# Kernel optimization log

Measured on AMD Instinct MI355X. Metric: run time of the kernel, lower is better.

Reference implementation:

```python
import jax, jax.numpy as jnp
import numpy as np

HIDDEN = 896
N_HEADS = 14
N_KV_HEADS = 2
HEAD_DIM = HIDDEN // N_HEADS  # 64
ROPE_THETA = 1000000.0
B, S = 2, 2048


def setup_inputs() -> dict:
    key = jax.random.key(0)
    ks = jax.random.split(key, 8)
    hidden_states = jax.random.normal(ks[0], (B, S, HIDDEN), dtype=jnp.float32)
    # causal additive mask (1,1,S,S): 0 allowed, -1e9 masked
    causal = jnp.tril(jnp.ones((S, S), dtype=bool))
    attention_mask = jnp.where(causal, 0.0, -1e9).astype(jnp.float32)[None, None]
    sc = 1.0 / np.sqrt(HIDDEN)
    Wq = jax.random.normal(ks[1], (N_HEADS * HEAD_DIM, HIDDEN), dtype=jnp.float32) * sc
    bq = jnp.zeros((N_HEADS * HEAD_DIM,), dtype=jnp.float32)
    Wk = jax.random.normal(ks[2], (N_KV_HEADS * HEAD_DIM, HIDDEN), dtype=jnp.float32) * sc
    bk = jnp.zeros((N_KV_HEADS * HEAD_DIM,), dtype=jnp.float32)
    Wv = jax.random.normal(ks[3], (N_KV_HEADS * HEAD_DIM, HIDDEN), dtype=jnp.float32) * sc
    bv = jnp.zeros((N_KV_HEADS * HEAD_DIM,), dtype=jnp.float32)
    Wo = jax.random.normal(ks[4], (HIDDEN, N_HEADS * HEAD_DIM), dtype=jnp.float32) * sc
    return {"hidden_states": hidden_states, "attention_mask": attention_mask,
            "Wq": Wq, "bq": bq, "Wk": Wk, "bk": bk, "Wv": Wv, "bv": bv, "Wo": Wo}


def _rotate_half(x):
    h = x.shape[-1] // 2
    return jnp.concatenate((-x[..., h:], x[..., :h]), axis=-1)


def _rope_cos_sin(seq_len, dtype):
    inv_freq = 1.0 / (ROPE_THETA ** (jnp.arange(0, HEAD_DIM, 2, dtype=jnp.float32) / HEAD_DIM))
    t = jnp.arange(seq_len, dtype=jnp.float32)
    freqs = jnp.outer(t, inv_freq)                 # [S, D/2]
    emb = jnp.concatenate((freqs, freqs), axis=-1)  # [S, D]
    return jnp.cos(emb).astype(dtype)[None, None], jnp.sin(emb).astype(dtype)[None, None]


def reference(hidden_states, attention_mask, Wq, bq, Wk, bk, Wv, bv, Wo):
    b, s, _ = hidden_states.shape
    groups = N_HEADS // N_KV_HEADS
    q = (hidden_states @ Wq.T + bq).reshape(b, s, N_HEADS, HEAD_DIM).transpose(0, 2, 1, 3)
    k = (hidden_states @ Wk.T + bk).reshape(b, s, N_KV_HEADS, HEAD_DIM).transpose(0, 2, 1, 3)
    v = (hidden_states @ Wv.T + bv).reshape(b, s, N_KV_HEADS, HEAD_DIM).transpose(0, 2, 1, 3)
    cos, sin = _rope_cos_sin(s, q.dtype)
    q = q * cos + _rotate_half(q) * sin
    k = k * cos + _rotate_half(k) * sin
    k = jnp.repeat(k, groups, axis=1)  # GQA expand: [b, H, s, d]
    v = jnp.repeat(v, groups, axis=1)
    scores = jnp.einsum('bhqd,bhkd->bhqk', q, k) / np.sqrt(HEAD_DIM) + attention_mask
    w = jax.nn.softmax(scores.astype(jnp.float32), axis=-1).astype(q.dtype)
    out = jnp.einsum('bhqk,bhkd->bhqd', w, v)
    out = out.transpose(0, 2, 1, 3).reshape(b, s, HIDDEN)
    return out @ Wo.T
```

## Files before the change

kernel.cpp:

```cpp
#include <hip/hip_runtime.h>
#include <hip/hip_bf16.h>

#define BATCH 2
#define SEQ   2048
#define HID   896
#define NH    14
#define NKV   2
#define HDIM  64
#define GRP   7
#define ROWS  (BATCH*SEQ)
#define NQKV  1152

typedef float f32x4 __attribute__((ext_vector_type(4)));
typedef short s16x8 __attribute__((ext_vector_type(8)));
typedef unsigned short u16;

#define MFMA_BF16(a,b,c) __builtin_amdgcn_mfma_f32_16x16x32_bf16((a),(b),(c),0,0,0)

__device__ __forceinline__ u16 f2b(float f) {
  __hip_bfloat16 h = __float2bfloat16(f);
  return __builtin_bit_cast(u16, h);
}
__device__ __forceinline__ float b2f(u16 u) {
  unsigned v = ((unsigned)u) << 16;
  return __builtin_bit_cast(float, v);
}

__device__ __forceinline__ void gload16(const void* g, void* l) {
  __builtin_amdgcn_global_load_lds((const __attribute__((address_space(1))) void*)g,
                                   (__attribute__((address_space(3))) void*)l,
                                   16, 0, 0);
}

__device__ __forceinline__ int chunk_prefix(int qi) {
  if (qi < 32)  return qi;
  if (qi < 64)  return 32 + (qi - 32) * 2;
  if (qi < 96)  return 96 + (qi - 64) * 3;
  return 192 + (qi - 96) * 4;
}

__global__ __launch_bounds__(256) void k_prep(const float* __restrict__ hidden,
                                              const float* __restrict__ Wq,
                                              const float* __restrict__ Wk,
                                              const float* __restrict__ Wv,
                                              const float* __restrict__ Wo,
                                              u16* __restrict__ hidB,
                                              u16* __restrict__ WqkvB,
                                              u16* __restrict__ WoB,
                                              float* __restrict__ ct,
                                              float* __restrict__ st) {
  const int bid = blockIdx.x, t = threadIdx.x;
  if (bid < 5376) {
    const float* src; u16* dst; int i;
    if (bid < 3584)      { src = hidden; dst = hidB;            i = bid*256 + t; }
    else if (bid < 4368) { src = Wq;     dst = WqkvB;           i = (bid-3584)*256 + t; }
    else if (bid < 4480) { src = Wk;     dst = WqkvB + 802816;  i = (bid-4368)*256 + t; }
    else if (bid < 4592) { src = Wv;     dst = WqkvB + 917504;  i = (bid-4480)*256 + t; }
    else                 { src = Wo;     dst = WoB;             i = (bid-4592)*256 + t; }
    float4 v = reinterpret_cast<const float4*>(src)[i];
    ushort4 o = { f2b(v.x), f2b(v.y), f2b(v.z), f2b(v.w) };
    reinterpret_cast<ushort4*>(dst)[i] = o;
  } else {
    const int i = (bid - 5376)*256 + t;
    const int s = i >> 5, fi = i & 31;
    double inv = exp(-(double)fi / 32.0 * log(1.0e6));
    double ang = (double)s * inv;
    ct[i] = (float)cos(ang);
    st[i] = (float)sin(ang);
  }
}

__global__ __launch_bounds__(256) void k_gemm_qkv(const u16* __restrict__ A,
                                                  const u16* __restrict__ Bt,
                                                  const float* __restrict__ bq,
                                                  const float* __restrict__ bk,
                                                  const float* __restrict__ bv,
                                                  const float* __restrict__ ct,
                                                  const float* __restrict__ st,
                                                  u16* __restrict__ Qr,
                                                  u16* __restrict__ Kf,
                                                  u16* __restrict__ Vf) {
  __shared__ __align__(16) u16 lA[2][128 * 32];
  __shared__ __align__(16) u16 lB[2][128 * 32];
  const int K = HID;
  const int t = threadIdx.x;
  const int l = t & 63, w = t >> 6;
  const int lr = l & 15, lg = l >> 4;
  const int wr = w >> 1, wc = w & 1;
  const int bm = blockIdx.x * 128, bn = blockIdx.y * 128;
  const int srow = (l >> 2) & 3;
  const int sslot = (l & 3) ^ srow;
  const int rsw = (lr & 3);

  f32x4 acc[4][4] = {};

#define GSTAGE(buf, k0)                                                          \
  {                                                                              \
    _Pragma("unroll")                                                            \
    for (int i = 0; i < 2; ++i) {                                                \
      const int row = i*64 + w*16 + (l>>2);                                      \
      gload16(A  + (size_t)(bm + row) * K + (k0) + sslot*8,                      \
              (char*)lA[buf] + i*4096 + w*1024);                                 \
      gload16(Bt + (size_t)(bn + row) * K + (k0) + sslot*8,                      \
              (char*)lB[buf] + i*4096 + w*1024);                                 \
    }                                                                            \
  }

  int cur = 0;
  GSTAGE(0, 0);
  __syncthreads();
  for (int k0 = 0; k0 < K; k0 += 32) {
    if (k0 + 32 < K) GSTAGE(cur ^ 1, k0 + 32);
    const u16* lAc = lA[cur];
    const u16* lBc = lB[cur];
    s16x8 af[4], bf[4];
    #pragma unroll
    for (int m = 0; m < 4; ++m)
      af[m] = *(const s16x8*)&lAc[(wr*64 + m*16 + lr)*32 + (lg ^ rsw)*8];
    #pragma unroll
    for (int n = 0; n < 4; ++n)
      bf[n] = *(const s16x8*)&lBc[(wc*64 + n*16 + lr)*32 + (lg ^ rsw)*8];
    #pragma unroll
    for (int m = 0; m < 4; ++m)
      #pragma unroll
      for (int n = 0; n < 4; ++n)
        acc[m][n] = MFMA_BF16(af[m], bf[n], acc[m][n]);
    __syncthreads();
    cur ^= 1;
  }
#undef GSTAGE

  const int hcol = blockIdx.y * 2 + wc;
  const int bsel = bm >> 11;
  const float QSC = 0.125f * 1.44269504088896f;

  if (hcol < 14) {
    u16* qb = Qr + (size_t)(bsel*NH + hcol) * SEQ * HDIM;
    float bia0[2], bia2[2];
    #pragma unroll
    for (int n = 0; n < 2; ++n) {
      bia0[n] = bq[hcol*64 + n*16 + lr];
      bia2[n] = bq[hcol*64 + n*16 + lr + 32];
    }
    #pragma unroll
    for (int m = 0; m < 4; ++m)
      #pragma unroll
      for (int j = 0; j < 4; ++j) {
        const int s = (bm + wr*64 + m*16 + lg*4 + j) & (SEQ - 1);
        #pragma unroll
        for (int n = 0; n < 2; ++n) {
          const int ic = n*16 + lr;
          const float c = ct[s*32 + ic], sv = st[s*32 + ic];
          const float x0 = acc[m][n][j] + bia0[n];
          const float x1 = acc[m][n+2][j] + bia2[n];
          qb[(size_t)s*HDIM + ic]      = f2b((x0*c - x1*sv) * QSC);
          qb[(size_t)s*HDIM + ic + 32] = f2b((x1*c + x0*sv) * QSC);
        }
      }
  } else if (hcol < 16) {
    const int hkk = hcol - 14;
    u16* kp = Kf + (size_t)(bsel*NKV + hkk) * SEQ * HDIM;
    float bia0[2], bia2[2];
    #pragma unroll
    for (int n = 0; n < 2; ++n) {
      bia0[n] = bk[hkk*64 + n*16 + lr];
      bia2[n] = bk[hkk*64 + n*16 + lr + 32];
    }
    #pragma unroll
    for (int m = 0; m < 4; ++m)
      #pragma unroll
      for (int j = 0; j < 4; ++j) {
        const int s = (bm + wr*64 + m*16 + lg*4 + j) & (SEQ - 1);
        #pragma unroll
        for (int n = 0; n < 2; ++n) {
          const int d0 = n*16 + lr;
          const float c = ct[s*32 + d0], sv = st[s*32 + d0];
          const float x0 = acc[m][n][j] + bia0[n];
          const float x1 = acc[m][n+2][j] + bia2[n];
          const int off0 = (s>>4)*1024 + ((d0>>3)*128) + (s&15)*8 + (d0&7);
          kp[off0]       = f2b(x0*c - x1*sv);
          kp[off0 + 512] = f2b(x1*c + x0*sv);
        }
      }
  } else {
    const int hkk = hcol - 16;
    u16* vp = Vf + (size_t)(bsel*NKV + hkk) * SEQ * HDIM;
    float biav[4];
    #pragma unroll
    for (int n = 0; n < 4; ++n) biav[n] = bv[hkk*64 + n*16 + lr];
    #pragma unroll
    for (int m = 0; m < 4; ++m)
      #pragma unroll
      for (int j = 0; j < 4; ++j) {
        const int s = (bm + wr*64 + m*16 + lg*4 + j) & (SEQ - 1);
        const int sbase = (s>>6)*4096 + ((s>>5)&1)*512 + ((s>>3)&3)*128 + (s&7);
        #pragma unroll
        for (int n = 0; n < 4; ++n)
          vp[sbase + n*1024 + lr*8] = f2b(acc[m][n][j] + biav[n]);
      }
  }
}

__global__ __launch_bounds__(256) void k_gemm_o(const u16* __restrict__ A,
                                                const u16* __restrict__ Bt,
                                                float* __restrict__ C,
                                                int N, int K) {
  __shared__ __align__(16) u16 lA[2][128 * 32];
  __shared__ __align__(16) u16 lB[2][128 * 32];
  const int t = threadIdx.x;
  const int l = t & 63, w = t >> 6;
  const int lr = l & 15, lg = l >> 4;
  const int wr = w >> 1, wc = w & 1;
  const int bm = blockIdx.x * 128, bn = blockIdx.y * 128;
  const int srow = (l >> 2) & 3;
  const int sslot = (l & 3) ^ srow;
  const int rsw = (lr & 3);

  f32x4 acc[4][4] = {};

#define GSTAGE(buf, k0)                                                          \
  {                                                                              \
    _Pragma("unroll")                                                            \
    for (int i = 0; i < 2; ++i) {                                                \
      const int row = i*64 + w*16 + (l>>2);                                      \
      gload16(A  + (size_t)(bm + row) * K + (k0) + sslot*8,                      \
              (char*)lA[buf] + i*4096 + w*1024);                                 \
      gload16(Bt + (size_t)(bn + row) * K + (k0) + sslot*8,                      \
              (char*)lB[buf] + i*4096 + w*1024);                                 \
    }                                                                            \
  }

  int cur = 0;
  GSTAGE(0, 0);
  __syncthreads();
  for (int k0 = 0; k0 < K; k0 += 32) {
    if (k0 + 32 < K) GSTAGE(cur ^ 1, k0 + 32);
    const u16* lAc = lA[cur];
    const u16* lBc = lB[cur];
    s16x8 af[4], bf[4];
    #pragma unroll
    for (int m = 0; m < 4; ++m)
      af[m] = *(const s16x8*)&lAc[(wr*64 + m*16 + lr)*32 + (lg ^ rsw)*8];
    #pragma unroll
    for (int n = 0; n < 4; ++n)
      bf[n] = *(const s16x8*)&lBc[(wc*64 + n*16 + lr)*32 + (lg ^ rsw)*8];
    #pragma unroll
    for (int m = 0; m < 4; ++m)
      #pragma unroll
      for (int n = 0; n < 4; ++n)
        acc[m][n] = MFMA_BF16(af[m], bf[n], acc[m][n]);
    __syncthreads();
    cur ^= 1;
  }
#undef GSTAGE

  #pragma unroll
  for (int n = 0; n < 4; ++n) {
    const int col = bn + wc*64 + n*16 + lr;
    #pragma unroll
    for (int m = 0; m < 4; ++m)
      #pragma unroll
      for (int j = 0; j < 4; ++j) {
        const int row = bm + wr*64 + m*16 + lg*4 + j;
        C[(size_t)row * N + col] = acc[m][n][j];
      }
  }
}

__global__ __launch_bounds__(256, 4) void k_attn(const u16* __restrict__ Qr,
                                                 const u16* __restrict__ Kf,
                                                 const u16* __restrict__ Vf,
                                                 u16* __restrict__ pAcc,
                                                 float* __restrict__ pML) {
  __shared__ __align__(16) u16 lP[4][16 * 64];

  const int t = threadIdx.x, l = t & 63, w = t >> 6;
  const int lr = l & 15, lg = l >> 4;
  const int g = blockIdx.x % 7;
  const int u = 319 - blockIdx.x / 7;
  int qi, ci;
  if (u < 32)       { qi = u;                 ci = 0; }
  else if (u < 96)  { qi = 32 + ((u-32)>>1);  ci = (u-32) & 1; }
  else if (u < 192) { const int v = u - 96;  const int q3 = v/3; qi = 64 + q3; ci = v - 3*q3; }
  else              { qi = 96 + ((u-192)>>2); ci = (u-192) & 3; }

  const int bh = g*4 + w;
  const int b = bh / NH, h = bh % NH, hk = h / GRP;
  const int nt = (qi >> 2) + 1;
  const int kt0 = ci * 8;
  const int kt1 = min(nt, kt0 + 8);
  const int dt = nt - 1;
  const int qloc = (qi & 3) * 16;
  const int task = bh*320 + chunk_prefix(qi) + ci;

  const u16* qbase = Qr + ((size_t)((b*NH + h) * SEQ + qi*16 + lr)) * HDIM + lg*8;
  const s16x8 qf0 = *(const s16x8*)qbase;
  const s16x8 qf1 = *(const s16x8*)(qbase + 32);
  const u16* kfp = Kf + (size_t)(b*NKV + hk) * SEQ * HDIM;
  const u16* vfp = Vf + (size_t)(b*NKV + hk) * SEQ * HDIM;

  f32x4 acc[4] = {};
  float lrow[4] = {0.f, 0.f, 0.f, 0.f};

  const int psw = (lr >> 2) << 4;

  for (int kt = kt0; kt < kt1; ++kt) {
    const u16* kbb = kfp + (size_t)kt*4096 + l*8;
    const s16x8 kf0 = *(const s16x8*)(kbb);
    const s16x8 kf1 = *(const s16x8*)(kbb + 512);
    const s16x8 kf2 = *(const s16x8*)(kbb + 1024);
    const s16x8 kf3 = *(const s16x8*)(kbb + 1536);
    const s16x8 kf4 = *(const s16x8*)(kbb + 2048);
    const s16x8 kf5 = *(const s16x8*)(kbb + 2560);
    const s16x8 kf6 = *(const s16x8*)(kbb + 3072);
    const s16x8 kf7 = *(const s16x8*)(kbb + 3584);

    f32x4 sc[4];
    __builtin_amdgcn_s_setprio(1);
    {
      f32x4 z0 = {0.f,0.f,0.f,0.f}, z1 = {0.f,0.f,0.f,0.f};
      f32x4 z2 = {0.f,0.f,0.f,0.f}, z3 = {0.f,0.f,0.f,0.f};
      z0 = MFMA_BF16(qf0, kf0, z0); z0 = MFMA_BF16(qf1, kf1, z0);
      z1 = MFMA_BF16(qf0, kf2, z1); z1 = MFMA_BF16(qf1, kf3, z1);
      z2 = MFMA_BF16(qf0, kf4, z2); z2 = MFMA_BF16(qf1, kf5, z2);
      z3 = MFMA_BF16(qf0, kf6, z3); z3 = MFMA_BF16(qf1, kf7, z3);
      sc[0] = z0; sc[1] = z1; sc[2] = z2; sc[3] = z3;
    }
    __builtin_amdgcn_s_setprio(0);

    const u16* vbb = vfp + (size_t)kt*4096 + l*8;
    const s16x8 vv0 = *(const s16x8*)(vbb);
    const s16x8 vv1 = *(const s16x8*)(vbb + 512);
    const s16x8 vv2 = *(const s16x8*)(vbb + 1024);
    const s16x8 vv3 = *(const s16x8*)(vbb + 1536);
    const s16x8 vv4 = *(const s16x8*)(vbb + 2048);
    const s16x8 vv5 = *(const s16x8*)(vbb + 2560);
    const s16x8 vv6 = *(const s16x8*)(vbb + 3072);
    const s16x8 vv7 = *(const s16x8*)(vbb + 3584);

    if (kt == dt) {
      #pragma unroll
      for (int f = 0; f < 4; ++f)
        #pragma unroll
        for (int j = 0; j < 4; ++j)
          if (f*16 + lr > qloc + lg*4 + j) sc[f][j] = -1.0e9f;
    }

    #pragma unroll
    for (int f = 0; f < 4; ++f)
      #pragma unroll
      for (int j = 0; j < 4; ++j) {
        float p = exp2f(sc[f][j]);
        sc[f][j] = p;
        lrow[j] += p;
      }

    u16* pw = lP[w];
    #pragma unroll
    for (int f = 0; f < 4; ++f)
      #pragma unroll
      for (int j = 0; j < 4; ++j)
        pw[(lg*4 + j)*64 + ((f*16 + lr) ^ (lg << 4))] = f2b(sc[f][j]);
    s16x8 pa0 = *(const s16x8*)&pw[lr*64 + ((lg*8     ) ^ psw)];
    s16x8 pa1 = *(const s16x8*)&pw[lr*64 + ((32 + lg*8) ^ psw)];

    __builtin_amdgcn_s_setprio(1);
    acc[0] = MFMA_BF16(pa0, vv0, acc[0]); acc[0] = MFMA_BF16(pa1, vv1, acc[0]);
    acc[1] = MFMA_BF16(pa0, vv2, acc[1]); acc[1] = MFMA_BF16(pa1, vv3, acc[1]);
    acc[2] = MFMA_BF16(pa0, vv4, acc[2]); acc[2] = MFMA_BF16(pa1, vv5, acc[2]);
    acc[3] = MFMA_BF16(pa0, vv6, acc[3]); acc[3] = MFMA_BF16(pa1, vv7, acc[3]);
    __builtin_amdgcn_s_setprio(0);
  }

  #pragma unroll
  for (int off = 1; off < 16; off <<= 1)
    #pragma unroll
    for (int j = 0; j < 4; ++j)
      lrow[j] += __shfl_xor(lrow[j], off);

  u16* pa = pAcc + (size_t)task * 1024;
  #pragma unroll
  for (int df = 0; df < 4; ++df) {
    ushort4 o = { f2b(acc[df][0]), f2b(acc[df][1]), f2b(acc[df][2]), f2b(acc[df][3]) };
    *reinterpret_cast<ushort4*>(pa + (df*64 + l)*4) = o;
  }
  if (lr == 0) {
    float* ml = pML + task * 32;
    #pragma unroll
    for (int j = 0; j < 4; ++j)
      ml[lg*4 + j] = lrow[j];
  }
}

__global__ __launch_bounds__(256) void k_reduce(const u16* __restrict__ pAcc,
                                                const float* __restrict__ pML,
                                                u16* __restrict__ Ao) {
  __shared__ __align__(16) u16 lT[4][16 * 64];
  const int t = threadIdx.x, l = t & 63, w = t >> 6;
  const int lr = l & 15, lg = l >> 4;
  const int id = blockIdx.x * 4 + w;
  const int qi = id & 127, bh = id >> 7;
  const int b = bh / NH, h = bh % NH;
  const int nch = 1 + (qi >> 5);
  const int base = bh*320 + chunk_prefix(qi);

  float inv[4];
  #pragma unroll
  for (int j = 0; j < 4; ++j) {
    const int r = lg*4 + j;
    const float l0 = pML[(size_t)(base+0)*32 + r];
    const float l1 = (nch > 1) ? pML[(size_t)(base+1)*32 + r] : 0.f;
    const float l2 = (nch > 2) ? pML[(size_t)(base+2)*32 + r] : 0.f;
    const float l3 = (nch > 3) ? pML[(size_t)(base+3)*32 + r] : 0.f;
    inv[j] = 1.0f / (l0 + l1 + l2 + l3);
  }

  u16* lt = lT[w];
  #pragma unroll
  for (int df = 0; df < 4; ++df) {
    const int eo = (df*64 + l)*4;
    ushort4 a0 = *reinterpret_cast<const ushort4*>(pAcc + (size_t)(base+0)*1024 + eo);
    ushort4 a1 = (nch > 1) ? *reinterpret_cast<const ushort4*>(pAcc + (size_t)(base+1)*1024 + eo) : ushort4{0,0,0,0};
    ushort4 a2 = (nch > 2) ? *reinterpret_cast<const ushort4*>(pAcc + (size_t)(base+2)*1024 + eo) : ushort4{0,0,0,0};
    ushort4 a3 = (nch > 3) ? *reinterpret_cast<const ushort4*>(pAcc + (size_t)(base+3)*1024 + eo) : ushort4{0,0,0,0};
    const u16 e0[4] = {a0.x, a0.y, a0.z, a0.w};
    const u16 e1[4] = {a1.x, a1.y, a1.z, a1.w};
    const u16 e2[4] = {a2.x, a2.y, a2.z, a2.w};
    const u16 e3[4] = {a3.x, a3.y, a3.z, a3.w};
    #pragma unroll
    for (int j = 0; j < 4; ++j) {
      float o = (b2f(e0[j]) + b2f(e1[j]) + b2f(e2[j]) + b2f(e3[j])) * inv[j];
      lt[(lg*4 + j)*64 + df*16 + lr] = f2b(o);
    }
  }

  const size_t orow = (size_t)b * SEQ + qi*16;
  #pragma unroll
  for (int i = 0; i < 2; ++i) {
    const int r = i*8 + (l >> 3);
    const s16x8 vrow = *(const s16x8*)&lt[r*64 + (l & 7)*8];
    *(s16x8*)&Ao[(orow + r) * HID + h*64 + (l & 7)*8] = vrow;
  }
}

extern "C" void kernel_launch(void* const* d_in, const int* in_sizes, int n_in,
                              void* d_out, int out_size, void* d_ws, size_t ws_size,
                              hipStream_t stream) {
  const float* hidden = (const float*)d_in[0];
  const float* Wq = (const float*)d_in[2];
  const float* bq = (const float*)d_in[3];
  const float* Wk = (const float*)d_in[4];
  const float* bk = (const float*)d_in[5];
  const float* Wv = (const float*)d_in[6];
  const float* bv = (const float*)d_in[7];
  const float* Wo = (const float*)d_in[8];

  char* ws = (char*)d_ws;
  u16*   hidB  = (u16*)(ws);
  u16*   Ao    = (u16*)(ws);
  u16*   WqkvB = (u16*)(ws + 7340032);
  u16*   WoB   = (u16*)(ws + 9404416);
  u16*   Qr    = (u16*)(ws + 11010048);
  u16*   Kf    = (u16*)(ws + 18350080);
  u16*   Vf    = (u16*)(ws + 19398656);
  float* ct    = (float*)(ws + 20447232);
  float* st    = (float*)(ws + 20709376);
  u16*   pAcc  = (u16*)(ws + 20971520);
  float* pML   = (float*)(ws + 39321600);

  k_prep<<<dim3(5632), dim3(256), 0, stream>>>(hidden, Wq, Wk, Wv, Wo,
                                               hidB, WqkvB, WoB, ct, st);
  k_gemm_qkv<<<dim3(32, 9), dim3(256), 0, stream>>>(hidB, WqkvB, bq, bk, bv,
                                                    ct, st, Qr, Kf, Vf);
  k_attn<<<dim3(2240), dim3(256), 0, stream>>>(Qr, Kf, Vf, pAcc, pML);
  k_reduce<<<dim3(896), dim3(256), 0, stream>>>(pAcc, pML, Ao);
  k_gemm_o<<<dim3(32, 7), dim3(256), 0, stream>>>(Ao, WoB, (float*)d_out, HID, HID);
}
```

Before: 104.3 us.

## Process two 16-row query tiles per wave in attention to reuse K/V loads

Each attention wave now handles 32 query rows (two 16-row MFMA tiles) instead of 16, so every K and V fragment loaded from global memory feeds twice as many MFMAs. The work decomposition, chunk prefix indexing, partial-accumulator layout and the reduce kernel are reworked for 32-row tiles, and the grids are halved. The cost is more registers (8 accumulators, double score fragments), a lower occupancy hint of 3, and fewer blocks to balance across CUs.

```diff
diff --git a/kernel.cpp b/kernel.cpp
--- a/kernel.cpp
+++ b/kernel.cpp
@@ -32,11 +32,15 @@
                                    16, 0, 0);
 }
 
-__device__ __forceinline__ int chunk_prefix(int qi) {
-  if (qi < 32)  return qi;
-  if (qi < 64)  return 32 + (qi - 32) * 2;
-  if (qi < 96)  return 96 + (qi - 64) * 3;
-  return 192 + (qi - 96) * 4;
+__device__ __forceinline__ int S8(int n) {
+  if (n <= 8)  return n;
+  if (n <= 16) return 2*n - 8;
+  if (n <= 24) return 3*n - 24;
+  return 4*n - 48;
+}
+__device__ __forceinline__ int prefJ(int qj) {
+  const int n = qj >> 1;
+  return 2*S8(n) + (qj & 1) * (1 + (n >> 3));
 }
 
 __global__ __launch_bounds__(256) void k_prep(const float* __restrict__ hidden,
@@ -267,40 +271,45 @@
   }
 }
 
-__global__ __launch_bounds__(256, 4) void k_attn(const u16* __restrict__ Qr,
+__global__ __launch_bounds__(256, 3) void k_attn(const u16* __restrict__ Qr,
                                                  const u16* __restrict__ Kf,
                                                  const u16* __restrict__ Vf,
                                                  u16* __restrict__ pAcc,
                                                  float* __restrict__ pML) {
-  __shared__ __align__(16) u16 lP[4][16 * 64];
+  __shared__ __align__(16) u16 lP[4][2048];
 
   const int t = threadIdx.x, l = t & 63, w = t >> 6;
   const int lr = l & 15, lg = l >> 4;
   const int g = blockIdx.x % 7;
-  const int u = 319 - blockIdx.x / 7;
-  int qi, ci;
-  if (u < 32)       { qi = u;                 ci = 0; }
-  else if (u < 96)  { qi = 32 + ((u-32)>>1);  ci = (u-32) & 1; }
-  else if (u < 192) { const int v = u - 96;  const int q3 = v/3; qi = 64 + q3; ci = v - 3*q3; }
-  else              { qi = 96 + ((u-192)>>2); ci = (u-192) & 3; }
+  const int u = 159 - blockIdx.x / 7;
+  int qj, ci;
+  if (u < 16)       { qj = u;                 ci = 0; }
+  else if (u < 48)  { qj = 16 + ((u-16)>>1);  ci = (u-16) & 1; }
+  else if (u < 96)  { const int v = u - 48; const int q3 = v/3; qj = 32 + q3; ci = v - 3*q3; }
+  else              { qj = 48 + ((u-96)>>2);  ci = (u-96) & 3; }
 
   const int bh = g*4 + w;
   const int b = bh / NH, h = bh % NH, hk = h / GRP;
-  const int nt = (qi >> 2) + 1;
+  const int nt = (qj >> 1) + 1;
   const int kt0 = ci * 8;
   const int kt1 = min(nt, kt0 + 8);
   const int dt = nt - 1;
-  const int qloc = (qi & 3) * 16;
-  const int task = bh*320 + chunk_prefix(qi) + ci;
-
-  const u16* qbase = Qr + ((size_t)((b*NH + h) * SEQ + qi*16 + lr)) * HDIM + lg*8;
-  const s16x8 qf0 = *(const s16x8*)qbase;
-  const s16x8 qf1 = *(const s16x8*)(qbase + 32);
+  const int qloc0 = (qj & 1) * 32;
+  const int task = bh*160 + prefJ(qj) + ci;
+
+  const u16* qb0 = Qr + ((size_t)((b*NH + h) * SEQ + qj*32 + lr)) * HDIM + lg*8;
+  const s16x8 qf00 = *(const s16x8*)qb0;
+  const s16x8 qf01 = *(const s16x8*)(qb0 + 32);
+  const u16* qb1 = qb0 + 16 * HDIM;
+  const s16x8 qf10 = *(const s16x8*)qb1;
+  const s16x8 qf11 = *(const s16x8*)(qb1 + 32);
+
   const u16* kfp = Kf + (size_t)(b*NKV + hk) * SEQ * HDIM;
   const u16* vfp = Vf + (size_t)(b*NKV + hk) * SEQ * HDIM;
 
-  f32x4 acc[4] = {};
-  float lrow[4] = {0.f, 0.f, 0.f, 0.f};
+  f32x4 acc[8] = {};
+  float lr0[4] = {0.f,0.f,0.f,0.f};
+  float lr1[4] = {0.f,0.f,0.f,0.f};
 
   const int psw = (lr >> 2) << 4;
 
@@ -315,16 +324,21 @@
     const s16x8 kf6 = *(const s16x8*)(kbb + 3072);
     const s16x8 kf7 = *(const s16x8*)(kbb + 3584);
 
-    f32x4 sc[4];
+    f32x4 sc0[4], sc1[4];
     __builtin_amdgcn_s_setprio(1);
     {
-      f32x4 z0 = {0.f,0.f,0.f,0.f}, z1 = {0.f,0.f,0.f,0.f};
-      f32x4 z2 = {0.f,0.f,0.f,0.f}, z3 = {0.f,0.f,0.f,0.f};
-      z0 = MFMA_BF16(qf0, kf0, z0); z0 = MFMA_BF16(qf1, kf1, z0);
-      z1 = MFMA_BF16(qf0, kf2, z1); z1 = MFMA_BF16(qf1, kf3, z1);
-      z2 = MFMA_BF16(qf0, kf4, z2); z2 = MFMA_BF16(qf1, kf5, z2);
-      z3 = MFMA_BF16(qf0, kf6, z3); z3 = MFMA_BF16(qf1, kf7, z3);
-      sc[0] = z0; sc[1] = z1; sc[2] = z2; sc[3] = z3;
+      f32x4 a0={0.f,0.f,0.f,0.f}, a1={0.f,0.f,0.f,0.f}, a2={0.f,0.f,0.f,0.f}, a3={0.f,0.f,0.f,0.f};
+      f32x4 b0={0.f,0.f,0.f,0.f}, b1={0.f,0.f,0.f,0.f}, b2={0.f,0.f,0.f,0.f}, b3={0.f,0.f,0.f,0.f};
+      a0 = MFMA_BF16(qf00, kf0, a0); a0 = MFMA_BF16(qf01, kf1, a0);
+      b0 = MFMA_BF16(qf10, kf0, b0); b0 = MFMA_BF16(qf11, kf1, b0);
+      a1 = MFMA_BF16(qf00, kf2, a1); a1 = MFMA_BF16(qf01, kf3, a1);
+      b1 = MFMA_BF16(qf10, kf2, b1); b1 = MFMA_BF16(qf11, kf3, b1);
+      a2 = MFMA_BF16(qf00, kf4, a2); a2 = MFMA_BF16(qf01, kf5, a2);
+      b2 = MFMA_BF16(qf10, kf4, b2); b2 = MFMA_BF16(qf11, kf5, b2);
+      a3 = MFMA_BF16(qf00, kf6, a3); a3 = MFMA_BF16(qf01, kf7, a3);
+      b3 = MFMA_BF16(qf10, kf6, b3); b3 = MFMA_BF16(qf11, kf7, b3);
+      sc0[0]=a0; sc0[1]=a1; sc0[2]=a2; sc0[3]=a3;
+      sc1[0]=b0; sc1[1]=b1; sc1[2]=b2; sc1[3]=b3;
     }
     __builtin_amdgcn_s_setprio(0);
 
@@ -342,101 +356,120 @@
       #pragma unroll
       for (int f = 0; f < 4; ++f)
         #pragma unroll
-        for (int j = 0; j < 4; ++j)
-          if (f*16 + lr > qloc + lg*4 + j) sc[f][j] = -1.0e9f;
+        for (int j = 0; j < 4; ++j) {
+          if (f*16 + lr > qloc0      + lg*4 + j) sc0[f][j] = -1.0e9f;
+          if (f*16 + lr > qloc0 + 16 + lg*4 + j) sc1[f][j] = -1.0e9f;
+        }
     }
 
     #pragma unroll
     for (int f = 0; f < 4; ++f)
       #pragma unroll
       for (int j = 0; j < 4; ++j) {
-        float p = exp2f(sc[f][j]);
-        sc[f][j] = p;
-        lrow[j] += p;
+        float p0 = exp2f(sc0[f][j]);
+        float p1 = exp2f(sc1[f][j]);
+        sc0[f][j] = p0; lr0[j] += p0;
+        sc1[f][j] = p1; lr1[j] += p1;
       }
 
     u16* pw = lP[w];
     #pragma unroll
     for (int f = 0; f < 4; ++f)
       #pragma unroll
-      for (int j = 0; j < 4; ++j)
-        pw[(lg*4 + j)*64 + ((f*16 + lr) ^ (lg << 4))] = f2b(sc[f][j]);
-    s16x8 pa0 = *(const s16x8*)&pw[lr*64 + ((lg*8     ) ^ psw)];
-    s16x8 pa1 = *(const s16x8*)&pw[lr*64 + ((32 + lg*8) ^ psw)];
+      for (int j = 0; j < 4; ++j) {
+        pw[(lg*4 + j)*64 + ((f*16 + lr) ^ (lg << 4))]        = f2b(sc0[f][j]);
+        pw[1024 + (lg*4 + j)*64 + ((f*16 + lr) ^ (lg << 4))] = f2b(sc1[f][j]);
+      }
+    const s16x8 pa00 = *(const s16x8*)&pw[lr*64 + ((lg*8     ) ^ psw)];
+    const s16x8 pa01 = *(const s16x8*)&pw[lr*64 + ((32 + lg*8) ^ psw)];
+    const s16x8 pa10 = *(const s16x8*)&pw[1024 + lr*64 + ((lg*8     ) ^ psw)];
+    const s16x8 pa11 = *(const s16x8*)&pw[1024 + lr*64 + ((32 + lg*8) ^ psw)];
 
     __builtin_amdgcn_s_setprio(1);
-    acc[0] = MFMA_BF16(pa0, vv0, acc[0]); acc[0] = MFMA_BF16(pa1, vv1, acc[0]);
-    acc[1] = MFMA_BF16(pa0, vv2, acc[1]); acc[1] = MFMA_BF16(pa1, vv3, acc[1]);
-    acc[2] = MFMA_BF16(pa0, vv4, acc[2]); acc[2] = MFMA_BF16(pa1, vv5, acc[2]);
-    acc[3] = MFMA_BF16(pa0, vv6, acc[3]); acc[3] = MFMA_BF16(pa1, vv7, acc[3]);
+    acc[0] = MFMA_BF16(pa00, vv0, acc[0]); acc[0] = MFMA_BF16(pa01, vv1, acc[0]);
+    acc[4] = MFMA_BF16(pa10, vv0, acc[4]); acc[4] = MFMA_BF16(pa11, vv1, acc[4]);
+    acc[1] = MFMA_BF16(pa00, vv2, acc[1]); acc[1] = MFMA_BF16(pa01, vv3, acc[1]);
+    acc[5] = MFMA_BF16(pa10, vv2, acc[5]); acc[5] = MFMA_BF16(pa11, vv3, acc[5]);
+    acc[2] = MFMA_BF16(pa00, vv4, acc[2]); acc[2] = MFMA_BF16(pa01, vv5, acc[2]);
+    acc[6] = MFMA_BF16(pa10, vv4, acc[6]); acc[6] = MFMA_BF16(pa11, vv5, acc[6]);
+    acc[3] = MFMA_BF16(pa00, vv6, acc[3]); acc[3] = MFMA_BF16(pa01, vv7, acc[3]);
+    acc[7] = MFMA_BF16(pa10, vv6, acc[7]); acc[7] = MFMA_BF16(pa11, vv7, acc[7]);
     __builtin_amdgcn_s_setprio(0);
   }
 
   #pragma unroll
   for (int off = 1; off < 16; off <<= 1)
     #pragma unroll
-    for (int j = 0; j < 4; ++j)
-      lrow[j] += __shfl_xor(lrow[j], off);
-
-  u16* pa = pAcc + (size_t)task * 1024;
+    for (int j = 0; j < 4; ++j) {
+      lr0[j] += __shfl_xor(lr0[j], off);
+      lr1[j] += __shfl_xor(lr1[j], off);
+    }
+
+  u16* pa = pAcc + (size_t)task * 2048;
   #pragma unroll
   for (int df = 0; df < 4; ++df) {
-    ushort4 o = { f2b(acc[df][0]), f2b(acc[df][1]), f2b(acc[df][2]), f2b(acc[df][3]) };
-    *reinterpret_cast<ushort4*>(pa + (df*64 + l)*4) = o;
+    ushort4 o0 = { f2b(acc[df][0]), f2b(acc[df][1]), f2b(acc[df][2]), f2b(acc[df][3]) };
+    ushort4 o1 = { f2b(acc[4+df][0]), f2b(acc[4+df][1]), f2b(acc[4+df][2]), f2b(acc[4+df][3]) };
+    *reinterpret_cast<ushort4*>(pa + (df*64 + l)*4)        = o0;
+    *reinterpret_cast<ushort4*>(pa + 1024 + (df*64 + l)*4) = o1;
   }
   if (lr == 0) {
     float* ml = pML + task * 32;
     #pragma unroll
-    for (int j = 0; j < 4; ++j)
-      ml[lg*4 + j] = lrow[j];
+    for (int j = 0; j < 4; ++j) {
+      ml[lg*4 + j]      = lr0[j];
+      ml[16 + lg*4 + j] = lr1[j];
+    }
   }
 }
 
 __global__ __launch_bounds__(256) void k_reduce(const u16* __restrict__ pAcc,
                                                 const float* __restrict__ pML,
                                                 u16* __restrict__ Ao) {
-  __shared__ __align__(16) u16 lT[4][16 * 64];
+  __shared__ __align__(16) u16 lT[4][2048];
   const int t = threadIdx.x, l = t & 63, w = t >> 6;
   const int lr = l & 15, lg = l >> 4;
   const int id = blockIdx.x * 4 + w;
-  const int qi = id & 127, bh = id >> 7;
+  const int qj = id & 63, bh = id >> 6;
   const int b = bh / NH, h = bh % NH;
-  const int nch = 1 + (qi >> 5);
-  const int base = bh*320 + chunk_prefix(qi);
-
-  float inv[4];
-  #pragma unroll
-  for (int j = 0; j < 4; ++j) {
-    const int r = lg*4 + j;
-    const float l0 = pML[(size_t)(base+0)*32 + r];
-    const float l1 = (nch > 1) ? pML[(size_t)(base+1)*32 + r] : 0.f;
-    const float l2 = (nch > 2) ? pML[(size_t)(base+2)*32 + r] : 0.f;
-    const float l3 = (nch > 3) ? pML[(size_t)(base+3)*32 + r] : 0.f;
-    inv[j] = 1.0f / (l0 + l1 + l2 + l3);
-  }
+  const int nch = 1 + (qj >> 4);
+  const int base = bh*160 + prefJ(qj);
 
   u16* lt = lT[w];
   #pragma unroll
-  for (int df = 0; df < 4; ++df) {
-    const int eo = (df*64 + l)*4;
-    ushort4 a0 = *reinterpret_cast<const ushort4*>(pAcc + (size_t)(base+0)*1024 + eo);
-    ushort4 a1 = (nch > 1) ? *reinterpret_cast<const ushort4*>(pAcc + (size_t)(base+1)*1024 + eo) : ushort4{0,0,0,0};
-    ushort4 a2 = (nch > 2) ? *reinterpret_cast<const ushort4*>(pAcc + (size_t)(base+2)*1024 + eo) : ushort4{0,0,0,0};
-    ushort4 a3 = (nch > 3) ? *reinterpret_cast<const ushort4*>(pAcc + (size_t)(base+3)*1024 + eo) : ushort4{0,0,0,0};
-    const u16 e0[4] = {a0.x, a0.y, a0.z, a0.w};
-    const u16 e1[4] = {a1.x, a1.y, a1.z, a1.w};
-    const u16 e2[4] = {a2.x, a2.y, a2.z, a2.w};
-    const u16 e3[4] = {a3.x, a3.y, a3.z, a3.w};
+  for (int frag = 0; frag < 2; ++frag) {
+    float inv[4];
     #pragma unroll
     for (int j = 0; j < 4; ++j) {
-      float o = (b2f(e0[j]) + b2f(e1[j]) + b2f(e2[j]) + b2f(e3[j])) * inv[j];
-      lt[(lg*4 + j)*64 + df*16 + lr] = f2b(o);
-    }
-  }
-
-  const size_t orow = (size_t)b * SEQ + qi*16;
+      const int r = frag*16 + lg*4 + j;
+      const float l0 = pML[(size_t)(base+0)*32 + r];
+      const float l1 = (nch > 1) ? pML[(size_t)(base+1)*32 + r] : 0.f;
+      const float l2 = (nch > 2) ? pML[(size_t)(base+2)*32 + r] : 0.f;
+      const float l3 = (nch > 3) ? pML[(size_t)(base+3)*32 + r] : 0.f;
+      inv[j] = 1.0f / (l0 + l1 + l2 + l3);
+    }
+    #pragma unroll
+    for (int df = 0; df < 4; ++df) {
+      const int eo = frag*1024 + (df*64 + l)*4;
+      ushort4 a0 = *reinterpret_cast<const ushort4*>(pAcc + (size_t)(base+0)*2048 + eo);
+      ushort4 a1 = (nch > 1) ? *reinterpret_cast<const ushort4*>(pAcc + (size_t)(base+1)*2048 + eo) : ushort4{0,0,0,0};
+      ushort4 a2 = (nch > 2) ? *reinterpret_cast<const ushort4*>(pAcc + (size_t)(base+2)*2048 + eo) : ushort4{0,0,0,0};
+      ushort4 a3 = (nch > 3) ? *reinterpret_cast<const ushort4*>(pAcc + (size_t)(base+3)*2048 + eo) : ushort4{0,0,0,0};
+      const u16 e0[4] = {a0.x, a0.y, a0.z, a0.w};
+      const u16 e1[4] = {a1.x, a1.y, a1.z, a1.w};
+      const u16 e2[4] = {a2.x, a2.y, a2.z, a2.w};
+      const u16 e3[4] = {a3.x, a3.y, a3.z, a3.w};
+      #pragma unroll
+      for (int j = 0; j < 4; ++j) {
+        float o = (b2f(e0[j]) + b2f(e1[j]) + b2f(e2[j]) + b2f(e3[j])) * inv[j];
+        lt[(frag*16 + lg*4 + j)*64 + df*16 + lr] = f2b(o);
+      }
+    }
+  }
+
+  const size_t orow = (size_t)b * SEQ + qj*32;
   #pragma unroll
-  for (int i = 0; i < 2; ++i) {
+  for (int i = 0; i < 4; ++i) {
     const int r = i*8 + (l >> 3);
     const s16x8 vrow = *(const s16x8*)&lt[r*64 + (l & 7)*8];
     *(s16x8*)&Ao[(orow + r) * HID + h*64 + (l & 7)*8] = vrow;
@@ -472,7 +505,7 @@
                                                hidB, WqkvB, WoB, ct, st);
   k_gemm_qkv<<<dim3(32, 9), dim3(256), 0, stream>>>(hidB, WqkvB, bq, bk, bv,
                                                     ct, st, Qr, Kf, Vf);
-  k_attn<<<dim3(2240), dim3(256), 0, stream>>>(Qr, Kf, Vf, pAcc, pML);
-  k_reduce<<<dim3(896), dim3(256), 0, stream>>>(pAcc, pML, Ao);
+  k_attn<<<dim3(1120), dim3(256), 0, stream>>>(Qr, Kf, Vf, pAcc, pML);
+  k_reduce<<<dim3(448), dim3(256), 0, stream>>>(pAcc, pML, Ao);
   k_gemm_o<<<dim3(32, 7), dim3(256), 0, stream>>>(Ao, WoB, (float*)d_out, HID, HID);
 }
```

Result: no change. 105.1 us (+0.7%).
